# Performance work log

Measured on AMD Instinct MI355X. Metric: run time of the kernel, lower is better.

Reference implementation:

```python
import jax, jax.numpy as jnp
import numpy as np

BETA = 0.01
EPS = 1e-6

def conv3x3(x, w, b):
    y = jax.lax.conv_general_dilated(x, w, (1, 1), 'SAME',
                                     dimension_numbers=('NCHW', 'OIHW', 'NCHW'))
    return y + b[None, :, None, None]

def variance_depth_flow(gt, patch, max_depth):
    B, C, H, W = gt.shape
    py, px = H // patch, W // patch
    # [B,C,py,px,P,P]
    p = gt.reshape(B, C, py, patch, px, patch).transpose(0, 1, 2, 4, 3, 5)
    p = jnp.where((p > 0.1) & (p < max_depth), p, jnp.zeros_like(p))
    bn = jnp.log(p[..., 0, :] + EPS)   # north border  [B,C,py,px,P]
    bs = jnp.log(p[..., -1, :] + EPS)  # south
    bw = jnp.log(p[..., :, 0] + EPS)   # west
    be = jnp.log(p[..., :, -1] + EPS)  # east
    def sx(b):  # shift patches left along x (axis=3), zero-pad last column
        return jnp.concatenate([b[:, :, :, 1:], jnp.zeros_like(b[:, :, :, :1])], axis=3)
    def sy(b):  # shift patches up along y (axis=2), zero-pad last row
        return jnp.concatenate([b[:, :, 1:], jnp.zeros_like(b[:, :, :1])], axis=2)
    diffs = [be - sx(bw), bs - sy(bn), be - sx(be), bs - sy(bs), bw - sx(bw),
             bn - sy(bn), bs - sx(bs), be - sy(be), bn - sx(bn), bw - sy(bw)]
    d = jnp.stack([x.sum(-1) for x in diffs], axis=-1)  # [B,C,py,px,10]
    d = d[:, 0].transpose(0, 3, 1, 2) / patch            # [B,10,py,px]
    return d

def smooth_l1(pred, target, beta):
    d = pred - target
    ad = jnp.abs(d)
    return jnp.where(ad < beta, 0.5 * d * d / beta, ad - 0.5 * beta)

def setup_inputs() -> dict:
    key = jax.random.key(0)
    ks = jax.random.split(key, 7)
    B, FC, DC, hw, HW = 32, 256, 64, 64, 512
    feat = jax.random.normal(ks[0], (B, FC, hw, hw), dtype=jnp.float32)
    depth = jax.random.normal(ks[1], (B, DC, hw, hw), dtype=jnp.float32)
    gts = jax.random.uniform(ks[2], (B, 1, HW, HW), dtype=jnp.float32)
    W_att = jax.random.normal(ks[3], (DC, FC, 3, 3), dtype=jnp.float32) * 0.02
    b_att = jnp.zeros((DC,), dtype=jnp.float32)
    W_post = jax.random.normal(ks[4], (10, DC, 3, 3), dtype=jnp.float32) * 0.05
    b_post = jnp.zeros((10,), dtype=jnp.float32)
    return {"feat": feat, "depth": depth, "gts": gts,
            "W_att": W_att, "b_att": b_att, "W_post": W_post, "b_post": b_post}

def reference(feat, depth, gts, W_att, b_att, W_post, b_post):
    max_depth = 80.0
    n, c, h, w = depth.shape
    patch = gts.shape[2] // h
    flow_gradient = variance_depth_flow(gts, patch, max_depth)  # [B,10,h,w]
    att = jax.nn.sigmoid(conv3x3(feat, W_att, b_att))           # [B,DC,h,w]
    ds = conv3x3(att * depth, W_post, b_post)                   # [B,10,h,w]
    diff = smooth_l1(ds, flow_gradient, BETA)
    return diff.sum() / (h * w * ds.shape[0] * ds.shape[1])
```

## Files before the change

### kernel.cpp

```cpp
#include <hip/hip_runtime.h>
#include <hip/hip_bf16.h>


typedef __attribute__((ext_vector_type(4))) float f32x4;
typedef __attribute__((ext_vector_type(8))) short s16x8;
typedef __attribute__((ext_vector_type(4))) unsigned int u32x4;

#define DEVFN __device__ __forceinline__

DEVFN float bf2f(unsigned short u){
  unsigned int x = ((unsigned int)u) << 16;
  float f; __builtin_memcpy(&f, &x, 4); return f;
}
DEVFN unsigned short f2bf(float f){
  unsigned int x; __builtin_memcpy(&x, &f, 4);
  x += 0x7fffu + ((x >> 16) & 1u);
  return (unsigned short)(x >> 16);
}
DEVFN unsigned cvtpk(float lo, float hi){
  unsigned r;
  asm("v_cvt_pk_bf16_f32 %0, %1, %2" : "=v"(r) : "v"(lo), "v"(hi));
  return r;
}

#define ASYNC16(gp, lp) __builtin_amdgcn_global_load_lds( \
    (const __attribute__((address_space(1))) unsigned int*)(gp), \
    (__attribute__((address_space(3))) unsigned int*)(lp), 16, 0, 0)

__global__ void k_weights(const float* __restrict__ Watt, const float* __restrict__ Wpost,
                          unsigned short* __restrict__ WT1, unsigned short* __restrict__ WT2){
  const int t = blockIdx.x * 256 + threadIdx.x;
  const int n1 = 9 * 64 * 256;
  if (t < n1){
    const int tap = t / (64 * 256);
    const int rem = t % (64 * 256);
    const int oc = rem / 256, ic = rem % 256;
    WT1[t] = f2bf(Watt[(oc * 256 + ic) * 9 + tap]);
  }
  const int n2 = 9 * 16 * 64;
  if (t < n2){
    const int tap = t / (16 * 64);
    const int rem = t % (16 * 64);
    const int od = rem / 64, ic = rem % 64;
    const float v = (od < 10) ? Wpost[(od * 64 + ic) * 9 + tap] : 0.0f;
    WT2[t] = f2bf(v);
  }
}

__global__ void k_borders(const float* __restrict__ gts, float* __restrict__ S,
                          float* __restrict__ out){
  const int bid = blockIdx.x, tid = threadIdx.x;
  if (bid == 0 && tid == 0) *out = 0.0f;
  __shared__ float slab[4096];
  const int rel = bid;
  const float* gp = gts + (size_t)rel * 4096;
#pragma unroll
  for (int it = 0; it < 4; ++it){
    const int id = it * 256 + tid;
    *(f32x4*)&slab[id * 4] = *(const f32x4*)&gp[id * 4];
  }
  __syncthreads();
  const int px = tid & 63, border = tid >> 6;
  float s = 0.0f;
#pragma unroll
  for (int i = 0; i < 8; ++i){
    float v;
    if (border == 0)      v = slab[px * 8 + i];
    else if (border == 1) v = slab[7 * 512 + px * 8 + i];
    else if (border == 2) v = slab[i * 512 + px * 8];
    else                  v = slab[i * 512 + px * 8 + 7];
    v = ((v > 0.1f) && (v < 80.0f)) ? v : 0.0f;
    s += __logf(v + 1e-6f);
  }
  S[((size_t)rel * 64 + px) * 4 + border] = s;
}

__global__ __launch_bounds__(256, 2) void k_gemm1(
    const float* __restrict__ feat,
    const unsigned short* __restrict__ WT1,
    const float* __restrict__ batt,
    const float* __restrict__ depth,
    unsigned short* __restrict__ adT)
{
  __shared__ unsigned short As[6 * 17 * 16 * 8];
  __shared__ unsigned short Bs[576 * 32];
  const int t = threadIdx.x;
  const int l = t & 63, w = t >> 6;
  const int b = blockIdx.x >> 4, ytile = blockIdx.x & 15;
  const int y0 = ytile * 4;
  const int fr = l & 15, g = l >> 4;

  f32x4 acc[4][4];
#pragma unroll
  for (int i = 0; i < 4; ++i)
#pragma unroll
    for (int j = 0; j < 4; ++j)
#pragma unroll
      for (int q = 0; q < 4; ++q) acc[i][j][q] = 0.0f;

  if (t < 96){
    const int yy = t >> 4, sp = t & 15;
    u32x4 z = {0, 0, 0, 0};
    *(u32x4*)&As[((yy * 17 + 16) * 16 + sp) * 8] = z;
  }

  auto loadRow = [&](int c, int yy, f32x4* v){
    const int yr = y0 - 1 + yy;
    if (yr >= 0 && yr < 64){
      const float* gp = feat + ((size_t)(b * 256 + c * 32 + g * 8)) * 4096
                             + (size_t)yr * 64 + fr * 4;
#pragma unroll
      for (int e = 0; e < 8; ++e) v[e] = *(const f32x4*)(gp + (size_t)e * 4096);
    } else {
#pragma unroll
      for (int e = 0; e < 8; ++e) v[e] = f32x4{0.f, 0.f, 0.f, 0.f};
    }
  };
  auto cvtWriteRow = [&](int yy, const f32x4* v){
#pragma unroll
    for (int o = 0; o < 4; ++o){
      u32x4 pk;
      pk[0] = cvtpk(v[0][o], v[1][o]);
      pk[1] = cvtpk(v[2][o], v[3][o]);
      pk[2] = cvtpk(v[4][o], v[5][o]);
      pk[3] = cvtpk(v[6][o], v[7][o]);
      const int sp = (4 * g + o) ^ fr;
      *(u32x4*)&As[((yy * 17 + fr) * 16 + sp) * 8] = pk;
    }
  };
  auto stageB = [&](int c){
#pragma unroll
    for (int it = 0; it < 9; ++it){
      const int idx = it * 256 + t;
      const int row = idx >> 2;
      const int sg = (idx & 3) ^ ((row >> 1) & 3);
      ASYNC16(WT1 + (size_t)row * 256 + c * 32 + sg * 8, &Bs[(size_t)idx * 8]);
    }
  };
  auto compute = [&](){
    const int slotB = (g ^ ((fr >> 1) & 3)) * 8;
#pragma unroll
    for (int tap = 0; tap < 9; ++tap){
      const int dy = tap / 3 - 1, dx = tap % 3 - 1;
      const int yy = w + dy + 1;
      const int rowb = yy * 17 * 16;
      s16x8 af[4], bfr[4];
#pragma unroll
      for (int i = 0; i < 4; ++i){
        const int x = i * 16 + fr + dx;
        const bool valid = (x >= 0) && (x < 64);
        const int xq = valid ? (x >> 2) : 16;
        const int sp = valid ? ((4 * g + (x & 3)) ^ (x >> 2)) : 4 * g;
        af[i] = *(const s16x8*)&As[(rowb + xq * 16 + sp) * 8];
      }
#pragma unroll
      for (int j = 0; j < 4; ++j)
        bfr[j] = *(const s16x8*)&Bs[(tap * 64 + j * 16 + fr) * 32 + slotB];
#pragma unroll
      for (int i = 0; i < 4; ++i)
#pragma unroll
        for (int j = 0; j < 4; ++j)
          acc[i][j] = __builtin_amdgcn_mfma_f32_16x16x32_bf16(af[i], bfr[j], acc[i][j], 0, 0, 0);
    }
  };

  f32x4 r0[8], r1[8];
  loadRow(0, w, r0);
  if (w < 2) loadRow(0, 4 + w, r1);
  stageB(0);
  cvtWriteRow(w, r0);
  if (w < 2) cvtWriteRow(4 + w, r1);
  __syncthreads();

  for (int c = 0; c < 8; ++c){
    if (c < 7){
      loadRow(c + 1, w, r0);
      if (w < 2) loadRow(c + 1, 4 + w, r1);
    }
    compute();
    __syncthreads();
    if (c < 7){
      cvtWriteRow(w, r0);
      if (w < 2) cvtWriteRow(4 + w, r1);
      stageB(c + 1);
    }
    __syncthreads();
  }

  const int y = y0 + w;
#pragma unroll
  for (int j = 0; j < 4; ++j){
    const int oc = j * 16 + fr;
    const float bb = batt[oc];
    const float* dpt = depth + ((size_t)(b * 64 + oc)) * 4096 + (size_t)y * 64;
    unsigned short* op = adT + ((size_t)(b * 4096 + y * 64)) * 64 + oc;
#pragma unroll
    for (int i = 0; i < 4; ++i){
      const f32x4 dv4 = *(const f32x4*)&dpt[i * 16 + g * 4];
#pragma unroll
      for (int q = 0; q < 4; ++q){
        const int xo = i * 16 + g * 4 + q;
        const float v = acc[i][j][q] + bb;
        const float att = 1.0f / (1.0f + __expf(-v));
        op[(size_t)xo * 64] = f2bf(att * dv4[q]);
      }
    }
  }
}

DEVFN float sel4(f32x4 v, int i){
  const float ab = (i & 1) ? v[1] : v[0];
  const float cd = (i & 1) ? v[3] : v[2];
  return (i & 2) ? cd : ab;
}

__global__ __launch_bounds__(512, 2) void k_gemm2(
    const unsigned short* __restrict__ adT,
    const unsigned short* __restrict__ WT2,
    const float* __restrict__ bpost,
    const f32x4* __restrict__ S,
    float* __restrict__ out)
{
  __shared__ unsigned short As[2][20480];
  __shared__ unsigned short Bs[9216];
  __shared__ float ps[8];
  const int t = threadIdx.x;
  const int l = t & 63, w = t >> 6;
  const int b = blockIdx.x >> 3, ytile = blockIdx.x & 7;
  const int y0 = ytile * 8;
  const int fr = l & 15, g = l >> 4;

  f32x4 acc[4];
#pragma unroll
  for (int i = 0; i < 4; ++i)
#pragma unroll
    for (int q = 0; q < 4; ++q) acc[i][q] = 0.0f;

  auto stageA = [&](int c, int d){
#pragma unroll
    for (int it2 = 0; it2 < 5; ++it2){
      const int it = it2 * 2 + (t >> 8);
      const int yy = y0 - 1 + it;
      const int xx = (t >> 2) & 63, icg = t & 3;
      unsigned short* lp = &As[d][(it * 64 + xx) * 32 + icg * 8];
      if (yy >= 0 && yy < 64){
        const int sg = icg ^ ((xx >> 1) & 3);
        const unsigned short* gp = adT
            + ((size_t)(b * 4096 + yy * 64 + xx)) * 64 + c * 32 + sg * 8;
        ASYNC16(gp, lp);
      } else {
        s16x8 z = {0,0,0,0,0,0,0,0};
        *(s16x8*)lp = z;
      }
    }
  };
#pragma unroll
  for (int it = 0; it < 3; ++it){
    const int idx = it * 512 + t;
    if (idx < 1152){
      const int row = idx >> 3, p = idx & 7;
      const int sg = p ^ (row & 7);
      ASYNC16(WT2 + (size_t)row * 64 + sg * 8, Bs + (size_t)idx * 8);
    }
  }
  stageA(0, 0);
  __syncthreads();

  for (int c = 0; c < 2; ++c){
    if (c == 0) stageA(1, 1);
    const unsigned short* Ab = As[c];
    const int pB = ((c * 4 + g) ^ (fr & 7)) * 8;
    for (int tap = 0; tap < 9; ++tap){
      const int dy = tap / 3 - 1, dx = tap % 3 - 1;
      s16x8 af[4];
#pragma unroll
      for (int i = 0; i < 4; ++i){
        const int xv = i * 16 + fr + dx;
        const bool valid = (xv >= 0) && (xv < 64);
        const int xw = valid ? xv : 0;
        const int slot = (g ^ ((xw >> 1) & 3)) * 8;
        s16x8 v = *(const s16x8*)&Ab[((w + dy + 1) * 64 + xw) * 32 + slot];
        s16x8 z = {0,0,0,0,0,0,0,0};
        af[i] = valid ? v : z;
      }
      const s16x8 bfr = *(const s16x8*)&Bs[(tap * 16 + fr) * 64 + pB];
#pragma unroll
      for (int i = 0; i < 4; ++i)
        acc[i] = __builtin_amdgcn_mfma_f32_16x16x32_bf16(af[i], bfr, acc[i], 0, 0, 0);
    }
    __syncthreads();
  }

  const unsigned aPack = (3u<<0)|(1u<<2)|(3u<<4)|(1u<<6)|(2u<<8)|(0u<<10)|(1u<<12)|(3u<<14)|(0u<<16)|(2u<<18);
  const unsigned bPack = (2u<<0)|(0u<<2)|(3u<<4)|(1u<<6)|(2u<<8)|(0u<<10)|(1u<<12)|(3u<<14)|(0u<<16)|(2u<<18);
  float lsum = 0.0f;
  const int y = y0 + w;
  if (fr < 10){
    const int od = fr;
    const int ai = (aPack >> (2 * od)) & 3;
    const int bi = (bPack >> (2 * od)) & 3;
    const bool xshift = (od & 1) == 0;
    const float bp = bpost[od];
#pragma unroll
    for (int i = 0; i < 4; ++i){
#pragma unroll
      for (int q = 0; q < 4; ++q){
        const int xo = i * 16 + g * 4 + q;
        const size_t gm = (size_t)b * 4096 + (size_t)y * 64 + xo;
        const f32x4 sa = S[gm];
        const bool nb = xshift ? (xo < 63) : (y < 63);
        const size_t ga = xshift ? (nb ? gm + 1 : gm) : (nb ? gm + 64 : gm);
        const f32x4 sbv = S[ga];
        const float sbf = nb ? sel4(sbv, bi) : 0.0f;
        const float flow = (sel4(sa, ai) - sbf) * 0.125f;
        const float dv = acc[i][q] + bp - flow;
        const float adv = fabsf(dv);
        lsum += (adv < 0.01f) ? (50.0f * dv * dv) : (adv - 0.005f);
      }
    }
  }
#pragma unroll
  for (int off = 32; off > 0; off >>= 1) lsum += __shfl_down(lsum, off);
  if (l == 0) ps[w] = lsum;
  __syncthreads();
  if (t == 0){
    float s = 0.0f;
#pragma unroll
    for (int i = 0; i < 8; ++i) s += ps[i];
    atomicAdd(out, s * (1.0f / 1310720.0f));
  }
}

extern "C" void kernel_launch(void* const* d_in, const int* in_sizes, int n_in,
                              void* d_out, int out_size, void* d_ws, size_t ws_size,
                              hipStream_t stream){
  const float* feat  = (const float*)d_in[0];
  const float* depth = (const float*)d_in[1];
  const float* gts   = (const float*)d_in[2];
  const float* Watt  = (const float*)d_in[3];
  const float* batt  = (const float*)d_in[4];
  const float* Wpost = (const float*)d_in[5];
  const float* bpost = (const float*)d_in[6];
  float* out = (float*)d_out;
  char* ws = (char*)d_ws;

  unsigned short* adT = (unsigned short*)ws;
  unsigned short* WT1 = (unsigned short*)(ws + 16777216);
  unsigned short* WT2 = (unsigned short*)(ws + 16777216 + 294912);
  float*          S   = (float*)(ws + 16777216 + 294912 + 18432);

  k_weights<<<576, 256, 0, stream>>>(Watt, Wpost, WT1, WT2);
  k_gemm1<<<512, 256, 0, stream>>>(feat, WT1, batt, depth, adT);
  k_borders<<<2048, 256, 0, stream>>>(gts, S, out);
  k_gemm2<<<256, 512, 0, stream>>>(adT, WT2, bpost, (const f32x4*)S, out);
}
```

Before: 88.20 us.

## Halve gemm1 row tile and split output channels across warps

The first conv GEMM now handles 2 output rows per block instead of 4, doubling the grid to 1024 blocks. The four warps are arranged as 2 rows by 2 output-channel halves, which halves each warp's accumulator count. The LDS swizzle for the feature tile is also redesigned. The aim is more blocks and better occupancy and latency hiding on a 256-CU part. The cost is a larger halo overhead, since 4 input rows are loaded for every 2 output rows instead of 6 for 4, and the weight slice is re-staged by twice as many blocks.

```diff
diff --git a/kernel.cpp b/kernel.cpp
--- a/kernel.cpp
+++ b/kernel.cpp
@@ -82,50 +82,52 @@
     const float* __restrict__ depth,
     unsigned short* __restrict__ adT)
 {
-  __shared__ unsigned short As[6 * 17 * 16 * 8];
+  __shared__ unsigned short As[4 * 17 * 16 * 8];
   __shared__ unsigned short Bs[576 * 32];
   const int t = threadIdx.x;
-  const int l = t & 63, w = t >> 6;
-  const int b = blockIdx.x >> 4, ytile = blockIdx.x & 15;
-  const int y0 = ytile * 4;
+  const int l = t & 63, wid = t >> 6;
+  const int wm = wid & 1, wo = wid >> 1;
+  const int b = blockIdx.x >> 5, ytile = blockIdx.x & 31;
+  const int y0 = ytile * 2;
   const int fr = l & 15, g = l >> 4;
 
-  f32x4 acc[4][4];
+  f32x4 acc[4][2];
 #pragma unroll
   for (int i = 0; i < 4; ++i)
 #pragma unroll
-    for (int j = 0; j < 4; ++j)
+    for (int j = 0; j < 2; ++j)
 #pragma unroll
       for (int q = 0; q < 4; ++q) acc[i][j][q] = 0.0f;
 
-  if (t < 96){
-    const int yy = t >> 4, sp = t & 15;
+  if (t < 64){
+    const int yy = t >> 4, u = t & 15;
     u32x4 z = {0, 0, 0, 0};
-    *(u32x4*)&As[((yy * 17 + 16) * 16 + sp) * 8] = z;
-  }
-
-  auto loadRow = [&](int c, int yy, f32x4* v){
-    const int yr = y0 - 1 + yy;
+    *(u32x4*)&As[((yy * 17 + 16) * 16 + u) * 8] = z;
+  }
+
+  f32x4 hold[8];
+  auto loadRow = [&](int c){
+    const int yr = y0 - 1 + wid;
     if (yr >= 0 && yr < 64){
       const float* gp = feat + ((size_t)(b * 256 + c * 32 + g * 8)) * 4096
                              + (size_t)yr * 64 + fr * 4;
 #pragma unroll
-      for (int e = 0; e < 8; ++e) v[e] = *(const f32x4*)(gp + (size_t)e * 4096);
+      for (int e = 0; e < 8; ++e) hold[e] = *(const f32x4*)(gp + (size_t)e * 4096);
     } else {
 #pragma unroll
-      for (int e = 0; e < 8; ++e) v[e] = f32x4{0.f, 0.f, 0.f, 0.f};
-    }
-  };
-  auto cvtWriteRow = [&](int yy, const f32x4* v){
+      for (int e = 0; e < 8; ++e) hold[e] = f32x4{0.f, 0.f, 0.f, 0.f};
+    }
+  };
+  auto cvtWriteRow = [&](){
 #pragma unroll
     for (int o = 0; o < 4; ++o){
       u32x4 pk;
-      pk[0] = cvtpk(v[0][o], v[1][o]);
-      pk[1] = cvtpk(v[2][o], v[3][o]);
-      pk[2] = cvtpk(v[4][o], v[5][o]);
-      pk[3] = cvtpk(v[6][o], v[7][o]);
-      const int sp = (4 * g + o) ^ fr;
-      *(u32x4*)&As[((yy * 17 + fr) * 16 + sp) * 8] = pk;
+      pk[0] = cvtpk(hold[0][o], hold[1][o]);
+      pk[1] = cvtpk(hold[2][o], hold[3][o]);
+      pk[2] = cvtpk(hold[4][o], hold[5][o]);
+      pk[3] = cvtpk(hold[6][o], hold[7][o]);
+      const int u = 4 * ((g ^ fr) & 3) + ((o ^ (fr >> 1)) & 3);
+      *(u32x4*)&As[((wid * 17 + fr) * 16 + u) * 8] = pk;
     }
   };
   auto stageB = [&](int c){
@@ -142,55 +144,49 @@
 #pragma unroll
     for (int tap = 0; tap < 9; ++tap){
       const int dy = tap / 3 - 1, dx = tap % 3 - 1;
-      const int yy = w + dy + 1;
+      const int yy = wm + dy + 1;
       const int rowb = yy * 17 * 16;
-      s16x8 af[4], bfr[4];
+      s16x8 af[4], bfr[2];
 #pragma unroll
       for (int i = 0; i < 4; ++i){
         const int x = i * 16 + fr + dx;
         const bool valid = (x >= 0) && (x < 64);
         const int xq = valid ? (x >> 2) : 16;
-        const int sp = valid ? ((4 * g + (x & 3)) ^ (x >> 2)) : 4 * g;
-        af[i] = *(const s16x8*)&As[(rowb + xq * 16 + sp) * 8];
-      }
-#pragma unroll
-      for (int j = 0; j < 4; ++j)
-        bfr[j] = *(const s16x8*)&Bs[(tap * 64 + j * 16 + fr) * 32 + slotB];
+        const int u = valid ? (4 * ((g ^ (x >> 2)) & 3) + (((x & 3) ^ (x >> 3)) & 3))
+                            : 4 * g;
+        af[i] = *(const s16x8*)&As[(rowb + xq * 16 + u) * 8];
+      }
+#pragma unroll
+      for (int j = 0; j < 2; ++j)
+        bfr[j] = *(const s16x8*)&Bs[(tap * 64 + wo * 32 + j * 16 + fr) * 32 + slotB];
 #pragma unroll
       for (int i = 0; i < 4; ++i)
 #pragma unroll
-        for (int j = 0; j < 4; ++j)
+        for (int j = 0; j < 2; ++j)
           acc[i][j] = __builtin_amdgcn_mfma_f32_16x16x32_bf16(af[i], bfr[j], acc[i][j], 0, 0, 0);
     }
   };
 
-  f32x4 r0[8], r1[8];
-  loadRow(0, w, r0);
-  if (w < 2) loadRow(0, 4 + w, r1);
+  loadRow(0);
   stageB(0);
-  cvtWriteRow(w, r0);
-  if (w < 2) cvtWriteRow(4 + w, r1);
+  cvtWriteRow();
   __syncthreads();
 
   for (int c = 0; c < 8; ++c){
-    if (c < 7){
-      loadRow(c + 1, w, r0);
-      if (w < 2) loadRow(c + 1, 4 + w, r1);
-    }
+    if (c < 7) loadRow(c + 1);
     compute();
     __syncthreads();
     if (c < 7){
-      cvtWriteRow(w, r0);
-      if (w < 2) cvtWriteRow(4 + w, r1);
+      cvtWriteRow();
       stageB(c + 1);
     }
     __syncthreads();
   }
 
-  const int y = y0 + w;
-#pragma unroll
-  for (int j = 0; j < 4; ++j){
-    const int oc = j * 16 + fr;
+  const int y = y0 + wm;
+#pragma unroll
+  for (int j = 0; j < 2; ++j){
+    const int oc = wo * 32 + j * 16 + fr;
     const float bb = batt[oc];
     const float* dpt = depth + ((size_t)(b * 64 + oc)) * 4096 + (size_t)y * 64;
     unsigned short* op = adT + ((size_t)(b * 4096 + y * 64)) * 64 + oc;
@@ -350,7 +346,7 @@
   float*          S   = (float*)(ws + 16777216 + 294912 + 18432);
 
   k_weights<<<576, 256, 0, stream>>>(Watt, Wpost, WT1, WT2);
-  k_gemm1<<<512, 256, 0, stream>>>(feat, WT1, batt, depth, adT);
+  k_gemm1<<<1024, 256, 0, stream>>>(feat, WT1, batt, depth, adT);
   k_borders<<<2048, 256, 0, stream>>>(gts, S, out);
   k_gemm2<<<256, 512, 0, stream>>>(adT, WT2, bpost, (const f32x4*)S, out);
 }
```

New measurement: 94.07 us. +6.7%, slower.
